# Kernel optimization log

Measured on AMD Instinct MI355X. Metric: run time of the kernel, lower is better.

The kernel has to match this reference:

```python
import jax, jax.numpy as jnp
import numpy as np

ANCHORS = jnp.array([[1.3221, 1.73145], [3.19275, 4.00944], [5.05587, 8.09892],
                     [9.47112, 4.84053], [11.2364, 10.0071]], dtype=jnp.float32)
NUM_ANCHORS = 5
NUM_CLASSES = 20
MAX_BOXES = 50
NOOBJECT_SCALE = 1.0
OBJECT_SCALE = 5.0
COORD_SCALE = 1.0
CLASS_SCALE = 1.0
SIL_THRESH = 0.6


def iou_cwh(b1, b2):
    # boxes as (cx, cy, w, h); matches repo bbox_ious(x1y1x2y2=False)
    x1, y1, w1, h1 = b1[..., 0], b1[..., 1], b1[..., 2], b1[..., 3]
    x2, y2, w2, h2 = b2[..., 0], b2[..., 1], b2[..., 2], b2[..., 3]
    uw = jnp.maximum(x1 + w1 * 0.5, x2 + w2 * 0.5) - jnp.minimum(x1 - w1 * 0.5, x2 - w2 * 0.5)
    uh = jnp.maximum(y1 + h1 * 0.5, y2 + h2 * 0.5) - jnp.minimum(y1 - h1 * 0.5, y2 - h2 * 0.5)
    cw = w1 + w2 - uw
    ch = h1 + h2 - uh
    inter = jnp.where((cw <= 0) | (ch <= 0), 0.0, cw * ch)
    return inter / (w1 * h1 + w2 * h2 - inter)


def setup_inputs() -> dict:
    key = jax.random.key(0)
    k1, k2, k3, k4 = jax.random.split(key, 4)
    nB = 64
    output = jax.random.normal(k1, (nB, NUM_ANCHORS * (5 + NUM_CLASSES), 38, 38), dtype=jnp.float32)
    # target layout per box: (class, x, y, w, h), all normalized; x>0 marks a valid box
    cls_col = jax.random.randint(k2, (nB, MAX_BOXES, 1), 0, NUM_CLASSES).astype(jnp.float32)
    xy = jax.random.uniform(k3, (nB, MAX_BOXES, 2), minval=0.05, maxval=0.95)
    wh = jax.random.uniform(k4, (nB, MAX_BOXES, 2), minval=0.02, maxval=0.3)
    target = jnp.concatenate([cls_col, xy, wh], axis=-1).reshape(nB, MAX_BOXES * 5)
    return {"output": output, "target": target}


def region_loss(output, target):
    nB = output.shape[0]
    nA, nC = NUM_ANCHORS, NUM_CLASSES
    nH, nW = output.shape[2], output.shape[3]
    out = output.reshape(nB, nA, 5 + nC, nH, nW)
    x = jax.nn.sigmoid(out[:, :, 0])
    y = jax.nn.sigmoid(out[:, :, 1])
    w = out[:, :, 2]
    h = out[:, :, 3]
    conf = jax.nn.sigmoid(out[:, :, 4])
    # [nB,nA,nC,nH,nW] -> [nB*nA*nH*nW, nC] (matches torch transpose/view order)
    cls_logits = jnp.transpose(out[:, :, 5:], (0, 1, 3, 4, 2)).reshape(-1, nC)

    sg = jax.lax.stop_gradient
    aw, ah = ANCHORS[:, 0], ANCHORS[:, 1]
    grid_x = jnp.arange(nW, dtype=jnp.float32)[None, None, None, :]
    grid_y = jnp.arange(nH, dtype=jnp.float32)[None, None, :, None]
    px = sg(x) + grid_x
    py = sg(y) + grid_y
    pw = jnp.exp(sg(w)) * aw[None, :, None, None]
    ph = jnp.exp(sg(h)) * ah[None, :, None, None]
    pred_boxes = jnp.stack([px, py, pw, ph], axis=-1)  # [nB,nA,nH,nW,4]

    # ---- build_targets (vectorized) ----
    tgt = sg(target).reshape(nB, MAX_BOXES, 5)
    gcls = tgt[:, :, 0]
    gx = tgt[:, :, 1] * nW
    gy = tgt[:, :, 2] * nH
    gw = tgt[:, :, 3] * nW
    gh = tgt[:, :, 4] * nH
    # loop breaks at first x==0 -> cumulative validity
    valid = jnp.cumprod((tgt[:, :, 1] != 0).astype(jnp.int32), axis=1).astype(bool)

    # silence conf_mask where any-GT IoU > thresh
    pb_flat = pred_boxes.reshape(nB, nA * nH * nW, 4)
    gt_boxes = jnp.stack([gx, gy, gw, gh], axis=-1)  # [nB,50,4]
    ious = iou_cwh(pb_flat[:, :, None, :], gt_boxes[:, None, :, :])  # [nB,nAnc,50]
    ious = jnp.where(valid[:, None, :], ious, 0.0)
    max_iou = jnp.max(ious, axis=2)
    conf_mask = jnp.where(max_iou > SIL_THRESH, 0.0, NOOBJECT_SCALE).reshape(nB, nA, nH, nW)

    # seen < 12800 defaults
    shp = (nB, nA, nH, nW)
    coord_mask = jnp.ones(shp, jnp.float32)
    tx = jnp.full(shp, 0.5, jnp.float32)
    ty = jnp.full(shp, 0.5, jnp.float32)
    tw = jnp.zeros(shp, jnp.float32)
    th = jnp.zeros(shp, jnp.float32)
    tconf = jnp.zeros(shp, jnp.float32)
    tcls = jnp.zeros(shp, jnp.float32)
    cls_mask = jnp.zeros(shp, jnp.float32)

    # best anchor per GT by (0,0,w,h) IoU; argmax keeps first max like the strict '>' loop
    zA = jnp.zeros_like(aw)
    anchor_boxes = jnp.stack([zA, zA, aw, ah], axis=-1)  # [nA,4]
    zg = jnp.zeros_like(gw)
    gt_wh = jnp.stack([zg, zg, gw, gh], axis=-1)  # [nB,50,4]
    a_iou = iou_cwh(gt_wh[:, :, None, :], anchor_boxes[None, None, :, :])  # [nB,50,nA]
    best_n = jnp.argmax(a_iou, axis=2)  # [nB,50]

    gi = jnp.clip(gx.astype(jnp.int32), 0, nW - 1)
    gj = jnp.clip(gy.astype(jnp.int32), 0, nH - 1)
    aw_b = aw[best_n]
    ah_b = ah[best_n]
    tx_v = gx - gi.astype(jnp.float32)
    ty_v = gy - gj.astype(jnp.float32)
    tw_v = jnp.log(gw / aw_b)
    th_v = jnp.log(gh / ah_b)
    b_ix = jnp.arange(nB)
    pred_at = pred_boxes[b_ix[:, None], best_n, gj, gi]  # [nB,50,4]
    iou_gt = iou_cwh(gt_boxes, pred_at)  # [nB,50]

    def step(carry, t):
        cm, clm, tx_, ty_, tw_, th_, tcf, tcl = carry
        bsel = jnp.where(valid[:, t], b_ix, nB)  # out-of-bounds -> dropped
        n, j, i = best_n[:, t], gj[:, t], gi[:, t]
        st = lambda a, v: a.at[bsel, n, j, i].set(v, mode='drop')
        cm = st(cm, jnp.full((nB,), OBJECT_SCALE, jnp.float32))
        clm = st(clm, jnp.ones((nB,), jnp.float32))
        tx_ = st(tx_, tx_v[:, t])
        ty_ = st(ty_, ty_v[:, t])
        tw_ = st(tw_, tw_v[:, t])
        th_ = st(th_, th_v[:, t])
        tcf = st(tcf, iou_gt[:, t])
        tcl = st(tcl, gcls[:, t])
        return (cm, clm, tx_, ty_, tw_, th_, tcf, tcl), None

    init = (conf_mask, cls_mask, tx, ty, tw, th, tconf, tcls)
    (conf_mask, cls_mask, tx, ty, tw, th, tconf, tcls), _ = jax.lax.scan(
        step, init, jnp.arange(MAX_BOXES))

    # ---- losses ----
    cmf = jnp.sqrt(conf_mask)
    loss_x = COORD_SCALE * jnp.sum((x * coord_mask - tx * coord_mask) ** 2) / 2.0
    loss_y = COORD_SCALE * jnp.sum((y * coord_mask - ty * coord_mask) ** 2) / 2.0
    loss_w = COORD_SCALE * jnp.sum((w * coord_mask - tw * coord_mask) ** 2) / 2.0
    loss_h = COORD_SCALE * jnp.sum((h * coord_mask - th * coord_mask) ** 2) / 2.0
    loss_conf = jnp.sum((conf * cmf - tconf * cmf) ** 2) / 2.0
    logp = jax.nn.log_softmax(cls_logits, axis=-1)
    labels = tcls.reshape(-1).astype(jnp.int32)
    ce = -jnp.take_along_axis(logp, labels[:, None], axis=1)[:, 0]
    loss_cls = CLASS_SCALE * jnp.sum(ce * cls_mask.reshape(-1))
    return loss_x + loss_y + loss_w + loss_h + loss_conf + loss_cls


def reference(output, target):
    return region_loss(output, target)
```

## Files before the change

### kernel.cpp

```cpp
#include <hip/hip_runtime.h>
#include <math.h>

#define NA 5
#define NC 20
#define NH 38
#define NW 38
#define MAX_BOXES 50
#define SPAT (NH * NW)
#define CELLS_PER_B (NA * SPAT)
#define TPB 256
#define WAVES 4
#define SLABS 113
#define GXB 29
#define WTOT (GXB * WAVES)
#define OBJECT_SCALE 5.0f
#define NOOBJECT_SCALE 1.0f

__constant__ float c_aw[NA]  = {1.3221f, 3.19275f, 5.05587f, 9.47112f, 11.2364f};
__constant__ float c_ah[NA]  = {1.73145f, 4.00944f, 8.09892f, 4.84053f, 10.0071f};
__constant__ float c_iaw[NA] = {1.f/1.3221f, 1.f/3.19275f, 1.f/5.05587f, 1.f/9.47112f, 1.f/11.2364f};
__constant__ float c_iah[NA] = {1.f/1.73145f, 1.f/4.00944f, 1.f/8.09892f, 1.f/4.84053f, 1.f/10.0071f};

__device__ __forceinline__ float fexp(float v) { return __expf(v); }
__device__ __forceinline__ float flog(float v) { return __logf(v); }
__device__ __forceinline__ float frcp(float v) { return __builtin_amdgcn_rcpf(v); }
__device__ __forceinline__ float fsig(float v) { return frcp(1.f + __expf(-v)); }

__device__ __forceinline__ void wave_lds_fence() {
  asm volatile("s_waitcnt lgkmcnt(0)" ::: "memory");
}

__device__ __forceinline__ float iou_fast(float x1, float y1, float w1, float h1,
                                          float x2, float y2, float w2, float h2) {
  float uw = fmaxf(x1 + w1 * 0.5f, x2 + w2 * 0.5f) - fminf(x1 - w1 * 0.5f, x2 - w2 * 0.5f);
  float uh = fmaxf(y1 + h1 * 0.5f, y2 + h2 * 0.5f) - fminf(y1 - h1 * 0.5f, y2 - h2 * 0.5f);
  float cw = w1 + w2 - uw;
  float ch = h1 + h2 - uh;
  float inter = (cw <= 0.f || ch <= 0.f) ? 0.f : cw * ch;
  return inter * frcp(w1 * h1 + w2 * h2 - inter);
}

__device__ __forceinline__ float iou_wh_exact(float w1, float h1, float w2, float h2) {
  float uw = fmaxf(w1 * 0.5f, w2 * 0.5f) - fminf(-w1 * 0.5f, -w2 * 0.5f);
  float uh = fmaxf(h1 * 0.5f, h2 * 0.5f) - fminf(-h1 * 0.5f, -h2 * 0.5f);
  float cw = w1 + w2 - uw;
  float ch = h1 + h2 - uh;
  float inter = (cw <= 0.f || ch <= 0.f) ? 0.f : cw * ch;
  return inter / (w1 * h1 + w2 * h2 - inter);
}

__global__ __launch_bounds__(TPB) void fused_kernel(
    const float* __restrict__ out, const float* __restrict__ target,
    float* __restrict__ partials) {
  const int b = blockIdx.y;
  const int wid = threadIdx.x >> 6;
  const int lane = threadIdx.x & 63;

  __shared__ float4 sb_lo[WAVES][MAX_BOXES];
  __shared__ float  sb_ag[WAVES][MAX_BOXES];

  if (blockIdx.x == 0 && wid == 0) {
    const int t = lane;
    float cls = 0.f, x = 0.f, y = 0.f, w = 0.f, h = 0.f;
    if (t < MAX_BOXES) {
      const float* tg = target + (size_t)(b * MAX_BOXES + t) * 5;
      cls = tg[0]; x = tg[1]; y = tg[2]; w = tg[3]; h = tg[4];
    }
    unsigned long long nz = __ballot(t < MAX_BOXES && x != 0.f);
    unsigned long long low = (t < 63) ? ((1ull << (t + 1)) - 1ull) : ~0ull;
    bool valid = (t < MAX_BOXES) && ((nz & low) == low);
    float gx = x * NW, gy = y * NH, gw = w * NW, gh = h * NH;

    int best = 0; float bestiou = -1.f;
#pragma unroll
    for (int a2 = 0; a2 < NA; ++a2) {
      float aiou = iou_wh_exact(gw, gh, c_aw[a2], c_ah[a2]);
      if (aiou > bestiou) { bestiou = aiou; best = a2; }
    }
    int gi = min(max((int)gx, 0), NW - 1);
    int gj = min(max((int)gy, 0), NH - 1);
    int cell = best * SPAT + gj * NW + gi;

    unsigned long long vm = __ballot(valid);
    bool winner = valid;
    for (int tp = 0; tp < MAX_BOXES; ++tp) {
      int c2 = __shfl(cell, tp);
      if (tp > t && ((vm >> tp) & 1ull) && c2 == cell) winner = false;
    }
    if (t < MAX_BOXES) {
      if (valid) {
        sb_lo[0][t] = make_float4(gx - gw * 0.5f, gx + gw * 0.5f, gy - gh * 0.5f, gy + gh * 0.5f);
        sb_ag[0][t] = 0.375f * (gw * gh);
      } else {
        sb_lo[0][t] = make_float4(1e30f, 1e30f, 1e30f, 1e30f);
        sb_ag[0][t] = 0.f;
      }
    }
    wave_lds_fence();

    float d = 0.f;
    if (winner) {
      const float* bp = out + ((size_t)(b * NA + best) * 25) * SPAT + gj * NW + gi;
      float v0 = bp[0], v1 = bp[SPAT], v2 = bp[2 * SPAT], v3 = bp[3 * SPAT], v4 = bp[4 * SPAT];
      float xs = fsig(v0), ys = fsig(v1), cs = fsig(v4);
      float pw = fexp(v2) * c_aw[best], ph = fexp(v3) * c_ah[best];
      float px = xs + (float)gi, py = ys + (float)gj;
      float plx = px - pw * 0.5f, phx = px + pw * 0.5f;
      float ply = py - ph * 0.5f, phy = py + ph * 0.5f;
      float ap = 0.375f * (pw * ph);

      float msc = -1e30f;
      for (int t2 = 0; t2 < MAX_BOXES; ++t2) {
        float4 l2 = sb_lo[0][t2];
        float cw = fminf(phx, l2.y) - fmaxf(plx, l2.x);
        float ch = fminf(phy, l2.w) - fmaxf(ply, l2.z);
        cw = fmaxf(cw, 0.f);
        msc = fmaxf(msc, fmaf(cw, ch, -sb_ag[0][t2]));
      }
      float cmask_def = (msc > ap) ? 0.f : NOOBJECT_SCALE;
      float xd = xs - 0.5f, yd = ys - 0.5f;
      float D = 0.5f * (xd * xd + yd * yd + v2 * v2 + v3 * v3 + cmask_def * (cs * cs));

      float txv = gx - (float)gi, tyv = gy - (float)gj;
      float twv = flog(gw * c_iaw[best]), thv = flog(gh * c_iah[best]);
      float tconf = iou_fast(gx, gy, gw, gh, px, py, pw, ph);
      float dx = xs - txv, dy = ys - tyv, dwv = v2 - twv, dhv = v3 - thv, dc = cs - tconf;

      int label = (int)cls;
      const float* cb = bp + 5 * SPAT;
      float m = -1e30f, lv = 0.f;
      for (int c = 0; c < NC; ++c) {
        float vvc = cb[c * SPAT];
        if (c == label) lv = vvc;
        m = fmaxf(m, vvc);
      }
      float ssum = 0.f;
      for (int c = 0; c < NC; ++c) ssum += fexp(cb[c * SPAT] - m);
      float ce = (m + flog(ssum)) - lv;

      float W = 0.5f * (dx * dx + dy * dy + dwv * dwv + dhv * dhv +
                        OBJECT_SCALE * (dc * dc)) + ce;
      d = W - D;
    }
    for (int o = 32; o > 0; o >>= 1) d += __shfl_down(d, o, 64);
    if (lane == 0) partials[(size_t)b * WTOT] = d;
    return;
  }

  const int slab = (blockIdx.x == 0) ? (wid - 1) : (3 + (blockIdx.x - 1) * WAVES + wid);
  const int s = slab * 64 + lane;
  const bool ok = (s < CELLS_PER_B);
  const int sc = ok ? s : 0;
  unsigned a = (unsigned)sc / SPAT;
  unsigned r = (unsigned)sc - a * SPAT;
  unsigned j = r / NW, i = r - j * NW;
  const float fi = (float)i, fj = (float)j;
  const float paw = c_aw[a], pah = c_ah[a];
  const float* bp = out + ((size_t)(b * NA + a) * 25) * SPAT + r;
  float v0 = bp[0], v1 = bp[SPAT], v2 = bp[2 * SPAT], v3 = bp[3 * SPAT], v4 = bp[4 * SPAT];

  {
    float x = 0.f, y = 0.f, w = 0.f, h = 0.f;
    if (lane < MAX_BOXES) {
      const float* tg = target + (size_t)(b * MAX_BOXES + lane) * 5;
      x = tg[1]; y = tg[2]; w = tg[3]; h = tg[4];
    }
    unsigned long long nz = __ballot(lane < MAX_BOXES && x != 0.f);
    unsigned long long low = (lane < 63) ? ((1ull << (lane + 1)) - 1ull) : ~0ull;
    bool valid = (lane < MAX_BOXES) && ((nz & low) == low);
    float gx = x * NW, gy = y * NH, gw = w * NW, gh = h * NH;
    if (lane < MAX_BOXES) {
      if (valid) {
        sb_lo[wid][lane] = make_float4(gx - gw * 0.5f, gx + gw * 0.5f, gy - gh * 0.5f, gy + gh * 0.5f);
        sb_ag[wid][lane] = 0.375f * (gw * gh);
      } else {
        sb_lo[wid][lane] = make_float4(1e30f, 1e30f, 1e30f, 1e30f);
        sb_ag[wid][lane] = 0.f;
      }
    }
  }

  float xs = fsig(v0), ys = fsig(v1), cs = fsig(v4);
  float pw = fexp(v2) * paw, ph = fexp(v3) * pah;
  float px = xs + fi, py = ys + fj;
  float plx = px - pw * 0.5f, phx = px + pw * 0.5f;
  float ply = py - ph * 0.5f, phy = py + ph * 0.5f;
  float ap = 0.375f * (pw * ph), msc = -1e30f;
  wave_lds_fence();

#pragma unroll
  for (int c0 = 0; c0 < MAX_BOXES; c0 += 5) {
    float4 bl[5]; float bag[5];
#pragma unroll
    for (int u = 0; u < 5; ++u) { bl[u] = sb_lo[wid][c0 + u]; bag[u] = sb_ag[wid][c0 + u]; }
#pragma unroll
    for (int u = 0; u < 5; ++u) {
      float cw = fminf(phx, bl[u].y) - fmaxf(plx, bl[u].x);
      float ch = fminf(phy, bl[u].w) - fmaxf(ply, bl[u].z);
      cw = fmaxf(cw, 0.f);
      msc = fmaxf(msc, fmaf(cw, ch, -bag[u]));
    }
  }

  float acc = 0.f;
  if (ok) {
    float cmask = (msc > ap) ? 0.f : NOOBJECT_SCALE;
    float xd = xs - 0.5f, yd = ys - 0.5f;
    acc = 0.5f * (xd * xd + yd * yd + v2 * v2 + v3 * v3 + cmask * (cs * cs));
  }
  for (int o = 32; o > 0; o >>= 1) acc += __shfl_down(acc, o, 64);
  if (lane == 0) partials[(size_t)b * WTOT + blockIdx.x * WAVES + wid] = acc;
}

__global__ __launch_bounds__(256) void reduce_kernel(
    const float* __restrict__ vals, int n, float* __restrict__ outv) {
  float acc = 0.f;
  for (int i = threadIdx.x; i < n; i += 256) acc += vals[i];
  for (int o = 32; o > 0; o >>= 1) acc += __shfl_down(acc, o, 64);
  __shared__ float s_red[4];
  int wid = threadIdx.x >> 6, lane = threadIdx.x & 63;
  if (lane == 0) s_red[wid] = acc;
  __syncthreads();
  if (threadIdx.x == 0) outv[0] = s_red[0] + s_red[1] + s_red[2] + s_red[3];
}

extern "C" void kernel_launch(void* const* d_in, const int* in_sizes, int n_in,
                              void* d_out, int out_size, void* d_ws, size_t ws_size,
                              hipStream_t stream) {
  const float* out = (const float*)d_in[0];
  const float* target = (const float*)d_in[1];
  int nB = in_sizes[0] / (NA * (5 + NC) * SPAT);

  float* partials = (float*)d_ws;

  hipLaunchKernelGGL(fused_kernel, dim3(GXB, nB), dim3(TPB), 0, stream,
                     out, target, partials);
  hipLaunchKernelGGL(reduce_kernel, dim3(1), dim3(256), 0, stream,
                     partials, WTOT * nB, (float*)d_out);
}
```

Before: 100.4 us.

## Process four cells per thread with float4 loads and shared box reads

Each lane now handles four consecutive spatial cells instead of one. It loads its five prediction channels as float4 vectors and runs the IoU max loop over all 50 ground-truth boxes for the four cells together, so each box value read from LDS is reused four times. The grid's x dimension shrinks from 29 to 8 blocks per batch to match the larger slabs. This reduces LDS traffic, load instruction count and wave launches, but leaves far fewer waves resident per CU, so there is less parallelism to hide memory latency. Register use also rises.

```diff
diff --git a/kernel.cpp b/kernel.cpp
--- a/kernel.cpp
+++ b/kernel.cpp
@@ -10,8 +10,10 @@
 #define CELLS_PER_B (NA * SPAT)
 #define TPB 256
 #define WAVES 4
-#define SLABS 113
-#define GXB 29
+#define CPT 4
+#define CPW (64 * CPT)
+#define SLABS ((CELLS_PER_B + CPW - 1) / CPW)
+#define GXB 8
 #define WTOT (GXB * WAVES)
 #define OBJECT_SCALE 5.0f
 #define NOOBJECT_SCALE 1.0f
@@ -148,16 +150,22 @@
   }
 
   const int slab = (blockIdx.x == 0) ? (wid - 1) : (3 + (blockIdx.x - 1) * WAVES + wid);
-  const int s = slab * 64 + lane;
-  const bool ok = (s < CELLS_PER_B);
-  const int sc = ok ? s : 0;
-  unsigned a = (unsigned)sc / SPAT;
-  unsigned r = (unsigned)sc - a * SPAT;
-  unsigned j = r / NW, i = r - j * NW;
-  const float fi = (float)i, fj = (float)j;
+  const int s0 = slab * CPW + lane * CPT;
+  const int sb = (s0 < CELLS_PER_B - CPT) ? s0 : (CELLS_PER_B - CPT);
+  const bool live = (slab < SLABS);
+  unsigned a = (unsigned)sb / SPAT;
+  unsigned r0 = (unsigned)sb - a * SPAT;
   const float paw = c_aw[a], pah = c_ah[a];
-  const float* bp = out + ((size_t)(b * NA + a) * 25) * SPAT + r;
-  float v0 = bp[0], v1 = bp[SPAT], v2 = bp[2 * SPAT], v3 = bp[3 * SPAT], v4 = bp[4 * SPAT];
+
+  float4 q0 = make_float4(0.f, 0.f, 0.f, 0.f), q1 = q0, q2 = q0, q3 = q0, q4 = q0;
+  if (live) {
+    const float* bp = out + ((size_t)(b * NA + a) * 25) * SPAT + r0;
+    q0 = *(const float4*)(bp);
+    q1 = *(const float4*)(bp + SPAT);
+    q2 = *(const float4*)(bp + 2 * SPAT);
+    q3 = *(const float4*)(bp + 3 * SPAT);
+    q4 = *(const float4*)(bp + 4 * SPAT);
+  }
 
   {
     float x = 0.f, y = 0.f, w = 0.f, h = 0.f;
@@ -180,12 +188,28 @@
     }
   }
 
-  float xs = fsig(v0), ys = fsig(v1), cs = fsig(v4);
-  float pw = fexp(v2) * paw, ph = fexp(v3) * pah;
-  float px = xs + fi, py = ys + fj;
-  float plx = px - pw * 0.5f, phx = px + pw * 0.5f;
-  float ply = py - ph * 0.5f, phy = py + ph * 0.5f;
-  float ap = 0.375f * (pw * ph), msc = -1e30f;
+  float v0[CPT] = {q0.x, q0.y, q0.z, q0.w};
+  float v1[CPT] = {q1.x, q1.y, q1.z, q1.w};
+  float v2[CPT] = {q2.x, q2.y, q2.z, q2.w};
+  float v3[CPT] = {q3.x, q3.y, q3.z, q3.w};
+  float v4[CPT] = {q4.x, q4.y, q4.z, q4.w};
+  float xs[CPT], ys[CPT], cs[CPT];
+  float plx[CPT], phx[CPT], ply[CPT], phy[CPT], ap[CPT], msc[CPT];
+#pragma unroll
+  for (int q = 0; q < CPT; ++q) {
+    unsigned r = r0 + q;
+    unsigned j = r / NW, i = r - j * NW;
+    float fi = (float)i, fj = (float)j;
+    xs[q] = fsig(v0[q]);
+    ys[q] = fsig(v1[q]);
+    cs[q] = fsig(v4[q]);
+    float pw = fexp(v2[q]) * paw, ph = fexp(v3[q]) * pah;
+    float px = xs[q] + fi, py = ys[q] + fj;
+    plx[q] = px - pw * 0.5f; phx[q] = px + pw * 0.5f;
+    ply[q] = py - ph * 0.5f; phy[q] = py + ph * 0.5f;
+    ap[q] = 0.375f * (pw * ph);
+    msc[q] = -1e30f;
+  }
   wave_lds_fence();
 
 #pragma unroll
@@ -195,18 +219,25 @@
     for (int u = 0; u < 5; ++u) { bl[u] = sb_lo[wid][c0 + u]; bag[u] = sb_ag[wid][c0 + u]; }
 #pragma unroll
     for (int u = 0; u < 5; ++u) {
-      float cw = fminf(phx, bl[u].y) - fmaxf(plx, bl[u].x);
-      float ch = fminf(phy, bl[u].w) - fmaxf(ply, bl[u].z);
-      cw = fmaxf(cw, 0.f);
-      msc = fmaxf(msc, fmaf(cw, ch, -bag[u]));
+#pragma unroll
+      for (int q = 0; q < CPT; ++q) {
+        float cw = fminf(phx[q], bl[u].y) - fmaxf(plx[q], bl[u].x);
+        float ch = fminf(phy[q], bl[u].w) - fmaxf(ply[q], bl[u].z);
+        cw = fmaxf(cw, 0.f);
+        msc[q] = fmaxf(msc[q], fmaf(cw, ch, -bag[u]));
+      }
     }
   }
 
   float acc = 0.f;
-  if (ok) {
-    float cmask = (msc > ap) ? 0.f : NOOBJECT_SCALE;
-    float xd = xs - 0.5f, yd = ys - 0.5f;
-    acc = 0.5f * (xd * xd + yd * yd + v2 * v2 + v3 * v3 + cmask * (cs * cs));
+#pragma unroll
+  for (int q = 0; q < CPT; ++q) {
+    bool ok = live && (s0 + q < CELLS_PER_B) && (s0 == sb);
+    if (!ok) continue;
+    float cmask = (msc[q] > ap[q]) ? 0.f : NOOBJECT_SCALE;
+    float xd = xs[q] - 0.5f, yd = ys[q] - 0.5f;
+    acc += 0.5f * (xd * xd + yd * yd + v2[q] * v2[q] + v3[q] * v3[q] +
+                   cmask * (cs[q] * cs[q]));
   }
   for (int o = 32; o > 0; o >>= 1) acc += __shfl_down(acc, o, 64);
   if (lane == 0) partials[(size_t)b * WTOT + blockIdx.x * WAVES + wid] = acc;
```

Result: no change. 99.71 us (-0.7%).
